# Optimization experiments

Hardware: AMD Instinct MI355X
Metric: run time of the kernel (lower is better)

## Reference

```python
import jax, jax.numpy as jnp
import numpy as np

BINS = 10
LOSS_WEIGHT = 1.0
N, C = 524288, 80


def setup_inputs() -> dict:
    key = jax.random.key(0)
    k1, k2 = jax.random.split(key)
    pred = jax.random.normal(k1, (N, C), dtype=jnp.float32)
    target = jax.random.randint(k2, (N, C), 0, 2).astype(jnp.float32)
    label_weight = jnp.ones((N, C), dtype=jnp.float32)
    return {"pred": pred, "target": target, "label_weight": label_weight}


def reference(pred, target, label_weight):
    # gradient magnitude g = |sigmoid(pred).detach() - target|, in [0, 1)
    g = jnp.abs(jax.nn.sigmoid(jax.lax.stop_gradient(pred)) - target)
    valid = (label_weight > 0)
    validf = valid.astype(pred.dtype)
    tot = jnp.maximum(jnp.sum(validf), 1.0)

    # edges[i] = i/BINS (last edge nudged by 1e-6) -> bin index = floor(g*BINS), clipped
    idx = jnp.clip(jnp.floor(g * BINS).astype(jnp.int32), 0, BINS - 1)
    counts = jnp.zeros((BINS,), dtype=pred.dtype).at[idx.ravel()].add(validf.ravel())
    nonempty = counts > 0
    n = jnp.sum(nonempty.astype(pred.dtype))

    w_per_bin = jnp.where(nonempty, tot / jnp.maximum(counts, 1.0), 0.0)
    weights = w_per_bin[idx] * validf
    weights = weights / jnp.maximum(n, 1.0)
    weights = jax.lax.stop_gradient(weights)  # weights carry no grad in the original

    # binary_cross_entropy_with_logits, elementwise, stable form
    bce = jnp.maximum(pred, 0.0) - pred * target + jnp.log1p(jnp.exp(-jnp.abs(pred)))
    loss = jnp.sum(weights * bce) / tot
    return loss * LOSS_WEIGHT
```

## Files before the change

kernel.cpp:

```cpp
#include <hip/hip_runtime.h>
#include <math.h>

#define BINS 10
#define NBLOCKS 2048
#define THREADS 256

struct Partial {
    float        sum[BINS];
    unsigned int cnt[BINS];
};

__device__ __forceinline__ void accum_one(float x, float t, float w,
                                          float (&s)[BINS], unsigned int (&c)[BINS]) {
    float ax  = __builtin_fabsf(x);
    float e   = __expf(-ax);
    float opd = 1.0f + e;
    float inv = __builtin_amdgcn_rcpf(opd);
    float sig = (x >= 0.0f) ? inv : (1.0f - inv);
    float g   = __builtin_fabsf(sig - t);
    int   idx = (int)(g * 10.0f);
    idx = idx > (BINS - 1) ? (BINS - 1) : idx;
    idx = (w > 0.0f) ? idx : -1;
    float bce = fmaxf(x, 0.0f) - x * t + __logf(opd);
#pragma unroll
    for (int b = 0; b < BINS; ++b) {
        bool m = (idx == b);
        s[b] += m ? bce : 0.0f;
        c[b] += (unsigned int)__popcll(__ballot(m));
    }
}

__global__ __launch_bounds__(THREADS) void ghmc_main(const float* __restrict__ pred,
                                                     const float* __restrict__ target,
                                                     const float* __restrict__ lw,
                                                     Partial* __restrict__ part,
                                                     long long total) {
    float        s[BINS];
    unsigned int c[BINS];
#pragma unroll
    for (int b = 0; b < BINS; ++b) { s[b] = 0.0f; c[b] = 0u; }

    const int tid = threadIdx.x;
    const long long nvec   = total >> 2;
    const long long stride = (long long)gridDim.x * THREADS;
    const float4* __restrict__ P = reinterpret_cast<const float4*>(pred);
    const float4* __restrict__ T = reinterpret_cast<const float4*>(target);
    const float4* __restrict__ W = reinterpret_cast<const float4*>(lw);

    long long i = (long long)blockIdx.x * THREADS + tid;
    for (; i + stride < nvec; i += 2 * stride) {
        float4 p0 = P[i];          float4 t0 = T[i];          float4 w0 = W[i];
        float4 p1 = P[i + stride]; float4 t1 = T[i + stride]; float4 w1 = W[i + stride];
        accum_one(p0.x, t0.x, w0.x, s, c);
        accum_one(p0.y, t0.y, w0.y, s, c);
        accum_one(p0.z, t0.z, w0.z, s, c);
        accum_one(p0.w, t0.w, w0.w, s, c);
        accum_one(p1.x, t1.x, w1.x, s, c);
        accum_one(p1.y, t1.y, w1.y, s, c);
        accum_one(p1.z, t1.z, w1.z, s, c);
        accum_one(p1.w, t1.w, w1.w, s, c);
    }
    for (; i < nvec; i += stride) {
        float4 p = P[i]; float4 t = T[i]; float4 w = W[i];
        accum_one(p.x, t.x, w.x, s, c);
        accum_one(p.y, t.y, w.y, s, c);
        accum_one(p.z, t.z, w.z, s, c);
        accum_one(p.w, t.w, w.w, s, c);
    }

    const long long base = nvec << 2;
    const int rem = (int)(total - base);
    if (blockIdx.x == 0 && tid < rem)
        accum_one(pred[base + tid], target[base + tid], lw[base + tid], s, c);

#pragma unroll
    for (int b = 0; b < BINS; ++b) {
#pragma unroll
        for (int off = 32; off; off >>= 1)
            s[b] += __shfl_xor(s[b], off, 64);
    }

    __shared__ float        ls[THREADS / 64][BINS];
    __shared__ unsigned int lc[THREADS / 64][BINS];
    const int wid  = tid >> 6;
    const int lane = tid & 63;
    if (lane == 0) {
#pragma unroll
        for (int b = 0; b < BINS; ++b) { ls[wid][b] = s[b]; lc[wid][b] = c[b]; }
    }
    __syncthreads();

    if (tid < BINS) {
        float sb = 0.0f; unsigned int cb = 0u;
#pragma unroll
        for (int w2 = 0; w2 < THREADS / 64; ++w2) { sb += ls[w2][tid]; cb += lc[w2][tid]; }
        part[blockIdx.x].sum[tid] = sb;
        part[blockIdx.x].cnt[tid] = cb;
    }
}

__global__ __launch_bounds__(THREADS) void ghmc_finalize(const Partial* __restrict__ part,
                                                         float* __restrict__ out,
                                                         int nblocks) {
    double             acc[BINS];
    unsigned long long cn[BINS];
#pragma unroll
    for (int b = 0; b < BINS; ++b) { acc[b] = 0.0; cn[b] = 0ull; }

    const int tid = threadIdx.x;
    for (int i = tid; i < nblocks; i += THREADS) {
#pragma unroll
        for (int b = 0; b < BINS; ++b) {
            acc[b] += (double)part[i].sum[b];
            cn[b]  += (unsigned long long)part[i].cnt[b];
        }
    }

#pragma unroll
    for (int b = 0; b < BINS; ++b) {
#pragma unroll
        for (int off = 32; off; off >>= 1) {
            acc[b] += __shfl_xor(acc[b], off, 64);
            cn[b]  += __shfl_xor(cn[b], off, 64);
        }
    }

    __shared__ double             lds_s[THREADS / 64][BINS];
    __shared__ unsigned long long lds_c[THREADS / 64][BINS];
    const int wid  = tid >> 6;
    const int lane = tid & 63;
    if (lane == 0) {
#pragma unroll
        for (int b = 0; b < BINS; ++b) { lds_s[wid][b] = acc[b]; lds_c[wid][b] = cn[b]; }
    }
    __syncthreads();

    if (tid == 0) {
        double loss = 0.0;
        int n = 0;
        for (int b = 0; b < BINS; ++b) {
            double sb = 0.0; unsigned long long cb = 0ull;
            for (int w2 = 0; w2 < THREADS / 64; ++w2) { sb += lds_s[w2][b]; cb += lds_c[w2][b]; }
            if (cb) { loss += sb / (double)cb; ++n; }
        }
        double denom = (n > 0) ? (double)n : 1.0;
        out[0] = (float)(loss / denom);
    }
}

extern "C" void kernel_launch(void* const* d_in, const int* in_sizes, int n_in,
                              void* d_out, int out_size, void* d_ws, size_t ws_size,
                              hipStream_t stream) {
    const float* pred   = (const float*)d_in[0];
    const float* target = (const float*)d_in[1];
    const float* lw     = (const float*)d_in[2];
    float* out = (float*)d_out;
    Partial* part = (Partial*)d_ws;
    const long long total = (long long)in_sizes[0];

    ghmc_main<<<NBLOCKS, THREADS, 0, stream>>>(pred, target, lw, part, total);
    ghmc_finalize<<<1, THREADS, 0, stream>>>(part, out, NBLOCKS);
}
```

Before: 449.0 us.

## Replace per-bin register masking with per-thread LDS histogram atomics

Each thread now keeps its own private slice of a shared-memory histogram and does two LDS atomic adds per element, indexed by bin. This replaces the unrolled 10-way compare, select and ballot/popcount per element. The goal is fewer VALU and scalar ops per element. In exchange it adds LDS traffic, 20 KB of LDS per block (which may reduce occupancy), and counts are now floats instead of integers, so per-thread counts lose exactness past 2^24.

Result: slower. 722.9 us (+61.0%).

```diff
diff --git a/kernel.cpp b/kernel.cpp
--- a/kernel.cpp
+++ b/kernel.cpp
@@ -6,12 +6,12 @@
 #define THREADS 256
 
 struct Partial {
-    float        sum[BINS];
-    unsigned int cnt[BINS];
+    float sum[BINS];
+    float cnt[BINS];
 };
 
 __device__ __forceinline__ void accum_one(float x, float t, float w,
-                                          float (&s)[BINS], unsigned int (&c)[BINS]) {
+                                          float* __restrict__ my) {
     float ax  = __builtin_fabsf(x);
     float e   = __expf(-ax);
     float opd = 1.0f + e;
@@ -20,14 +20,10 @@
     float g   = __builtin_fabsf(sig - t);
     int   idx = (int)(g * 10.0f);
     idx = idx > (BINS - 1) ? (BINS - 1) : idx;
-    idx = (w > 0.0f) ? idx : -1;
+    bool valid = (w > 0.0f);
     float bce = fmaxf(x, 0.0f) - x * t + __logf(opd);
-#pragma unroll
-    for (int b = 0; b < BINS; ++b) {
-        bool m = (idx == b);
-        s[b] += m ? bce : 0.0f;
-        c[b] += (unsigned int)__popcll(__ballot(m));
-    }
+    atomicAdd(&my[idx * THREADS],                  valid ? bce : 0.0f);
+    atomicAdd(&my[idx * THREADS + BINS * THREADS], valid ? 1.0f : 0.0f);
 }
 
 __global__ __launch_bounds__(THREADS) void ghmc_main(const float* __restrict__ pred,
@@ -35,12 +31,13 @@
                                                      const float* __restrict__ lw,
                                                      Partial* __restrict__ part,
                                                      long long total) {
-    float        s[BINS];
-    unsigned int c[BINS];
+    __shared__ float hist[2 * BINS * THREADS];
+    const int tid = threadIdx.x;
+    float* my = &hist[tid];
+
 #pragma unroll
-    for (int b = 0; b < BINS; ++b) { s[b] = 0.0f; c[b] = 0u; }
+    for (int b = 0; b < 2 * BINS; ++b) hist[b * THREADS + tid] = 0.0f;
 
-    const int tid = threadIdx.x;
     const long long nvec   = total >> 2;
     const long long stride = (long long)gridDim.x * THREADS;
     const float4* __restrict__ P = reinterpret_cast<const float4*>(pred);
@@ -51,49 +48,62 @@
     for (; i + stride < nvec; i += 2 * stride) {
         float4 p0 = P[i];          float4 t0 = T[i];          float4 w0 = W[i];
         float4 p1 = P[i + stride]; float4 t1 = T[i + stride]; float4 w1 = W[i + stride];
-        accum_one(p0.x, t0.x, w0.x, s, c);
-        accum_one(p0.y, t0.y, w0.y, s, c);
-        accum_one(p0.z, t0.z, w0.z, s, c);
-        accum_one(p0.w, t0.w, w0.w, s, c);
-        accum_one(p1.x, t1.x, w1.x, s, c);
-        accum_one(p1.y, t1.y, w1.y, s, c);
-        accum_one(p1.z, t1.z, w1.z, s, c);
-        accum_one(p1.w, t1.w, w1.w, s, c);
+        accum_one(p0.x, t0.x, w0.x, my);
+        accum_one(p0.y, t0.y, w0.y, my);
+        accum_one(p0.z, t0.z, w0.z, my);
+        accum_one(p0.w, t0.w, w0.w, my);
+        accum_one(p1.x, t1.x, w1.x, my);
+        accum_one(p1.y, t1.y, w1.y, my);
+        accum_one(p1.z, t1.z, w1.z, my);
+        accum_one(p1.w, t1.w, w1.w, my);
     }
     for (; i < nvec; i += stride) {
         float4 p = P[i]; float4 t = T[i]; float4 w = W[i];
-        accum_one(p.x, t.x, w.x, s, c);
-        accum_one(p.y, t.y, w.y, s, c);
-        accum_one(p.z, t.z, w.z, s, c);
-        accum_one(p.w, t.w, w.w, s, c);
+        accum_one(p.x, t.x, w.x, my);
+        accum_one(p.y, t.y, w.y, my);
+        accum_one(p.z, t.z, w.z, my);
+        accum_one(p.w, t.w, w.w, my);
     }
 
     const long long base = nvec << 2;
     const int rem = (int)(total - base);
     if (blockIdx.x == 0 && tid < rem)
-        accum_one(pred[base + tid], target[base + tid], lw[base + tid], s, c);
+        accum_one(pred[base + tid], target[base + tid], lw[base + tid], my);
 
+    __syncthreads();
+
+    float s[BINS], c[BINS];
+#pragma unroll
+    for (int b = 0; b < BINS; ++b) {
+        s[b] = hist[b * THREADS + tid];
+        c[b] = hist[b * THREADS + tid + BINS * THREADS];
+    }
 #pragma unroll
     for (int b = 0; b < BINS; ++b) {
 #pragma unroll
-        for (int off = 32; off; off >>= 1)
+        for (int off = 32; off; off >>= 1) {
             s[b] += __shfl_xor(s[b], off, 64);
+            c[b] += __shfl_xor(c[b], off, 64);
+        }
     }
-
-    __shared__ float        ls[THREADS / 64][BINS];
-    __shared__ unsigned int lc[THREADS / 64][BINS];
+    __syncthreads();
     const int wid  = tid >> 6;
     const int lane = tid & 63;
     if (lane == 0) {
 #pragma unroll
-        for (int b = 0; b < BINS; ++b) { ls[wid][b] = s[b]; lc[wid][b] = c[b]; }
+        for (int b = 0; b < BINS; ++b) {
+            hist[wid * BINS + b]                       = s[b];
+            hist[wid * BINS + b + (THREADS / 64) * BINS] = c[b];
+        }
     }
     __syncthreads();
-
     if (tid < BINS) {
-        float sb = 0.0f; unsigned int cb = 0u;
+        float sb = 0.0f, cb = 0.0f;
 #pragma unroll
-        for (int w2 = 0; w2 < THREADS / 64; ++w2) { sb += ls[w2][tid]; cb += lc[w2][tid]; }
+        for (int w2 = 0; w2 < THREADS / 64; ++w2) {
+            sb += hist[w2 * BINS + tid];
+            cb += hist[w2 * BINS + tid + (THREADS / 64) * BINS];
+        }
         part[blockIdx.x].sum[tid] = sb;
         part[blockIdx.x].cnt[tid] = cb;
     }
@@ -102,20 +112,18 @@
 __global__ __launch_bounds__(THREADS) void ghmc_finalize(const Partial* __restrict__ part,
                                                          float* __restrict__ out,
                                                          int nblocks) {
-    double             acc[BINS];
-    unsigned long long cn[BINS];
+    double acc[BINS], cn[BINS];
 #pragma unroll
-    for (int b = 0; b < BINS; ++b) { acc[b] = 0.0; cn[b] = 0ull; }
+    for (int b = 0; b < BINS; ++b) { acc[b] = 0.0; cn[b] = 0.0; }
 
     const int tid = threadIdx.x;
     for (int i = tid; i < nblocks; i += THREADS) {
 #pragma unroll
         for (int b = 0; b < BINS; ++b) {
             acc[b] += (double)part[i].sum[b];
-            cn[b]  += (unsigned long long)part[i].cnt[b];
+            cn[b]  += (double)part[i].cnt[b];
         }
     }
-
 #pragma unroll
     for (int b = 0; b < BINS; ++b) {
 #pragma unroll
@@ -125,8 +133,8 @@
         }
     }
 
-    __shared__ double             lds_s[THREADS / 64][BINS];
-    __shared__ unsigned long long lds_c[THREADS / 64][BINS];
+    __shared__ double lds_s[THREADS / 64][BINS];
+    __shared__ double lds_c[THREADS / 64][BINS];
     const int wid  = tid >> 6;
     const int lane = tid & 63;
     if (lane == 0) {
@@ -139,9 +147,9 @@
         double loss = 0.0;
         int n = 0;
         for (int b = 0; b < BINS; ++b) {
-            double sb = 0.0; unsigned long long cb = 0ull;
+            double sb = 0.0, cb = 0.0;
             for (int w2 = 0; w2 < THREADS / 64; ++w2) { sb += lds_s[w2][b]; cb += lds_c[w2][b]; }
-            if (cb) { loss += sb / (double)cb; ++n; }
+            if (cb > 0.0) { loss += sb / cb; ++n; }
         }
         double denom = (n > 0) ? (double)n : 1.0;
         out[0] = (float)(loss / denom);
```
